# Performance work log

Hardware: AMD Instinct MI355X
Metric: run time of the kernel (lower is better)

Reference implementation:

```python
import jax, jax.numpy as jnp
import numpy as np

K = 3       # kernel_size
SIGMA = 0.1 # noise scale


def setup_inputs() -> dict:
    key = jax.random.key(0)
    k1, k2 = jax.random.split(key)
    img = jax.random.uniform(k1, (32, 3, 512, 512), dtype=jnp.float32)
    noise = jax.random.normal(k2, (32, K, K), dtype=jnp.float32)
    return {"img": img, "noise": noise}


def reference(img, noise):
    b, c, h, w = img.shape
    # delta impulse: note original uses center = ceil(k/2) -> index 2 for k=3
    center = int(np.ceil(K / 2))
    delta = jnp.zeros((K, K), dtype=img.dtype).at[center, center].set(1.0)
    weight = (SIGMA * noise + delta)[:, None, :, :]  # [b, 1, K, K]
    x = jnp.transpose(img, (1, 0, 2, 3))  # [c, b, h, w]: conv batch=c, channels=b
    y = jax.lax.conv_general_dilated(
        x, weight,
        window_strides=(1, 1), padding='SAME',
        dimension_numbers=('NCHW', 'OIHW', 'NCHW'),
        feature_group_count=b,
    )  # [c, b, h, w]
    y = jnp.where(jnp.isnan(y), jnp.asarray(1.0, y.dtype), y)
    y = jnp.transpose(y, (1, 0, 2, 3))  # back to [b, c, h, w]
    return jnp.clip(y, 0.0, 1.0)
```

## Files before the change

### kernel.cpp

```cpp
#include <hip/hip_runtime.h>


#define RF_H 512
#define RF_W 512
#define RF_C 3
#define RF_PLANES 96
#define RF_SIGMA 0.1f
#define RF_W4 128
#define RF_STRIPS 128

__global__ __launch_bounds__(256) void RandomFilter_40767829574170_kernel(
    const float* __restrict__ img,
    const float* __restrict__ noise,
    float* __restrict__ out)
{
    const int idx   = blockIdx.x * 256 + threadIdx.x;
    const int w4    = idx & (RF_W4 - 1);
    const int strip = (idx >> 7) & (RF_STRIPS - 1);
    const int plane = idx >> 14;
    const int b     = plane / RF_C;

    const float* np_ = noise + b * 9;
    float wgt[3][3];
    #pragma unroll
    for (int r = 0; r < 3; ++r)
        #pragma unroll
        for (int s = 0; s < 3; ++s)
            wgt[r][s] = RF_SIGMA * np_[r * 3 + s];
    wgt[2][2] += 1.0f;

    const float* P  = img + plane * (RF_H * RF_W);
    const int    w0 = w4 * 4;
    const int    h0 = strip * 4;

    float L[6][6];
    #pragma unroll
    for (int r = 0; r < 6; ++r) {
        const int hr = h0 - 1 + r;
        if (hr < 0 || hr >= RF_H) {
            #pragma unroll
            for (int j = 0; j < 6; ++j) L[r][j] = 0.0f;
        } else {
            const float* row = P + (hr << 9);
            const float4 m = *reinterpret_cast<const float4*>(row + w0);
            L[r][1] = m.x; L[r][2] = m.y; L[r][3] = m.z; L[r][4] = m.w;
            L[r][0] = (w0 > 0)            ? row[w0 - 1] : 0.0f;
            L[r][5] = (w0 + 4 < RF_W)     ? row[w0 + 4] : 0.0f;
        }
    }

    float* outP = out + plane * (RF_H * RF_W) + w0;
    #pragma unroll
    for (int o = 0; o < 4; ++o) {
        float a0 = 0.f, a1 = 0.f, a2 = 0.f, a3 = 0.f;
        #pragma unroll
        for (int r = 0; r < 3; ++r) {
            const float k0 = wgt[r][0], k1 = wgt[r][1], k2 = wgt[r][2];
            a0 += k0 * L[o + r][0] + k1 * L[o + r][1] + k2 * L[o + r][2];
            a1 += k0 * L[o + r][1] + k1 * L[o + r][2] + k2 * L[o + r][3];
            a2 += k0 * L[o + r][2] + k1 * L[o + r][3] + k2 * L[o + r][4];
            a3 += k0 * L[o + r][3] + k1 * L[o + r][4] + k2 * L[o + r][5];
        }
        float4 ov;
        float* op = &ov.x;
        float  av[4] = {a0, a1, a2, a3};
        #pragma unroll
        for (int j = 0; j < 4; ++j) {
            float y = av[j];
            y = isnan(y) ? 1.0f : y;
            y = fminf(fmaxf(y, 0.0f), 1.0f);
            op[j] = y;
        }
        *reinterpret_cast<float4*>(outP + ((h0 + o) << 9)) = ov;
    }
}

extern "C" void kernel_launch(void* const* d_in, const int* in_sizes, int n_in,
                              void* d_out, int out_size, void* d_ws, size_t ws_size,
                              hipStream_t stream) {
    const float* img   = (const float*)d_in[0];
    const float* noise = (const float*)d_in[1];
    float* out = (float*)d_out;

    const int grid = RF_PLANES * RF_STRIPS * RF_W4 / 256;
    RandomFilter_40767829574170_kernel<<<grid, 256, 0, stream>>>(img, noise, out);
}
```

Measured before the change: 39.49 us.

## Use full-row wavefront tiles with rolling row window and shuffle halos

New measurement: 42.46 us. 1.08x slower.

```diff
diff --git a/kernel.cpp b/kernel.cpp
--- a/kernel.cpp
+++ b/kernel.cpp
@@ -3,22 +3,42 @@
 
 #define RF_H 512
 #define RF_W 512
-#define RF_C 3
-#define RF_PLANES 96
 #define RF_SIGMA 0.1f
-#define RF_W4 128
-#define RF_STRIPS 128
+
+typedef float floatx4 __attribute__((ext_vector_type(4)));
+
+__device__ __forceinline__ void build_win(floatx4 Bv, floatx4 Cv,
+                                          float mA, float mD, float zf,
+                                          float* w) {
+    const float left  = __shfl_up(Cv.w, 1);
+    const float right = __shfl_down(Bv.x, 1);
+    w[0] = left * mA * zf;
+    w[1] = Bv.x * zf; w[2] = Bv.y * zf; w[3] = Bv.z * zf; w[4] = Bv.w * zf;
+    w[5] = Cv.x * zf; w[6] = Cv.y * zf; w[7] = Cv.z * zf; w[8] = Cv.w * zf;
+    w[9] = right * mD * zf;
+}
 
 __global__ __launch_bounds__(256) void RandomFilter_40767829574170_kernel(
     const float* __restrict__ img,
     const float* __restrict__ noise,
     float* __restrict__ out)
 {
-    const int idx   = blockIdx.x * 256 + threadIdx.x;
-    const int w4    = idx & (RF_W4 - 1);
-    const int strip = (idx >> 7) & (RF_STRIPS - 1);
-    const int plane = idx >> 14;
-    const int b     = plane / RF_C;
+    const int tid   = threadIdx.x;
+    const int lane  = tid & 63;
+    const int wave  = tid >> 6;
+    const int plane = blockIdx.x >> 4;
+    const int band  = ((blockIdx.x & 15) << 2) | wave;
+    const int h0    = band << 3;
+    const int b     = plane / 3;
+
+    const float* P = img + plane * (RF_H * RF_W);
+    float*       O = out + plane * (RF_H * RF_W);
+    const int    w0 = lane << 3;
+
+    const float mA = (lane > 0)  ? 1.0f : 0.0f;
+    const float mD = (lane < 63) ? 1.0f : 0.0f;
+    const float ztop = (h0 == 0)          ? 0.0f : 1.0f;
+    const float zbot = (h0 + 8 == RF_H)   ? 0.0f : 1.0f;
 
     const float* np_ = noise + b * 9;
     float wgt[3][3];
@@ -29,50 +49,58 @@
             wgt[r][s] = RF_SIGMA * np_[r * 3 + s];
     wgt[2][2] += 1.0f;
 
-    const float* P  = img + plane * (RF_H * RF_W);
-    const int    w0 = w4 * 4;
-    const int    h0 = strip * 4;
-
-    float L[6][6];
-    #pragma unroll
-    for (int r = 0; r < 6; ++r) {
-        const int hr = h0 - 1 + r;
-        if (hr < 0 || hr >= RF_H) {
-            #pragma unroll
-            for (int j = 0; j < 6; ++j) L[r][j] = 0.0f;
-        } else {
-            const float* row = P + (hr << 9);
-            const float4 m = *reinterpret_cast<const float4*>(row + w0);
-            L[r][1] = m.x; L[r][2] = m.y; L[r][3] = m.z; L[r][4] = m.w;
-            L[r][0] = (w0 > 0)            ? row[w0 - 1] : 0.0f;
-            L[r][5] = (w0 + 4 < RF_W)     ? row[w0 + 4] : 0.0f;
-        }
+#define LOADROW(hr, Bv, Cv)                                                   \
+    {                                                                         \
+        const int hrc = (hr) < 0 ? 0 : ((hr) > RF_H - 1 ? RF_H - 1 : (hr));   \
+        const float* row_ = P + (hrc << 9);                                   \
+        Bv = *reinterpret_cast<const floatx4*>(row_ + w0);                    \
+        Cv = *reinterpret_cast<const floatx4*>(row_ + w0 + 4);                \
     }
 
-    float* outP = out + plane * (RF_H * RF_W) + w0;
+    floatx4 aB, aC, bB, bC, pB, pC, nB, nC;
+    LOADROW(h0 - 1, aB, aC);
+    LOADROW(h0,     bB, bC);
+    LOADROW(h0 + 1, pB, pC);
+    __builtin_amdgcn_sched_barrier(0);
+
+    float W[3][10];
+    build_win(aB, aC, mA, mD, ztop, W[0]);
+    build_win(bB, bC, mA, mD, 1.0f, W[1]);
+
     #pragma unroll
-    for (int o = 0; o < 4; ++o) {
-        float a0 = 0.f, a1 = 0.f, a2 = 0.f, a3 = 0.f;
+    for (int k = 0; k < 8; ++k) {
+        if (k < 7) { LOADROW(h0 + k + 2, nB, nC); }
+        __builtin_amdgcn_sched_barrier(0);
+
+        const float zf = (k == 7) ? zbot : 1.0f;
+        build_win(pB, pC, mA, mD, zf, W[(k + 2) % 3]);
+        pB = nB; pC = nC;
+
+        const float* Wm = W[k % 3];
+        const float* Wc = W[(k + 1) % 3];
+        const float* Wp = W[(k + 2) % 3];
+        float acc[8];
         #pragma unroll
-        for (int r = 0; r < 3; ++r) {
-            const float k0 = wgt[r][0], k1 = wgt[r][1], k2 = wgt[r][2];
-            a0 += k0 * L[o + r][0] + k1 * L[o + r][1] + k2 * L[o + r][2];
-            a1 += k0 * L[o + r][1] + k1 * L[o + r][2] + k2 * L[o + r][3];
-            a2 += k0 * L[o + r][2] + k1 * L[o + r][3] + k2 * L[o + r][4];
-            a3 += k0 * L[o + r][3] + k1 * L[o + r][4] + k2 * L[o + r][5];
+        for (int j = 0; j < 8; ++j) {
+            acc[j] = wgt[0][0] * Wm[j] + wgt[0][1] * Wm[j + 1] + wgt[0][2] * Wm[j + 2]
+                   + wgt[1][0] * Wc[j] + wgt[1][1] * Wc[j + 1] + wgt[1][2] * Wc[j + 2]
+                   + wgt[2][0] * Wp[j] + wgt[2][1] * Wp[j + 1] + wgt[2][2] * Wp[j + 2];
         }
-        float4 ov;
-        float* op = &ov.x;
-        float  av[4] = {a0, a1, a2, a3};
-        #pragma unroll
-        for (int j = 0; j < 4; ++j) {
-            float y = av[j];
-            y = isnan(y) ? 1.0f : y;
-            y = fminf(fmaxf(y, 0.0f), 1.0f);
-            op[j] = y;
-        }
-        *reinterpret_cast<float4*>(outP + ((h0 + o) << 9)) = ov;
+
+        floatx4 lo, hi;
+        lo.x = fminf(fmaxf(acc[0], 0.0f), 1.0f);
+        lo.y = fminf(fmaxf(acc[1], 0.0f), 1.0f);
+        lo.z = fminf(fmaxf(acc[2], 0.0f), 1.0f);
+        lo.w = fminf(fmaxf(acc[3], 0.0f), 1.0f);
+        hi.x = fminf(fmaxf(acc[4], 0.0f), 1.0f);
+        hi.y = fminf(fmaxf(acc[5], 0.0f), 1.0f);
+        hi.z = fminf(fmaxf(acc[6], 0.0f), 1.0f);
+        hi.w = fminf(fmaxf(acc[7], 0.0f), 1.0f);
+        float* orow = O + ((h0 + k) << 9) + w0;
+        *reinterpret_cast<floatx4*>(orow)     = lo;
+        *reinterpret_cast<floatx4*>(orow + 4) = hi;
     }
+#undef LOADROW
 }
 
 extern "C" void kernel_launch(void* const* d_in, const int* in_sizes, int n_in,
@@ -82,6 +110,5 @@
     const float* noise = (const float*)d_in[1];
     float* out = (float*)d_out;
 
-    const int grid = RF_PLANES * RF_STRIPS * RF_W4 / 256;
-    RandomFilter_40767829574170_kernel<<<grid, 256, 0, stream>>>(img, noise, out);
+    RandomFilter_40767829574170_kernel<<<1536, 256, 0, stream>>>(img, noise, out);
 }
```
